# Kernel optimization log

Hardware: AMD Instinct MI355X
Metric: run time of the kernel (lower is better)

## Reference

```python
import jax, jax.numpy as jnp
import numpy as np

N = 20000
IN_C = 512
HID = 64
H1 = 8
OUT_C = 256
E = 320000
NEG_SLOPE = 0.2


def gat_conv(x, src, dst, W, a_src, a_dst, b, concat):
    # PyG GATConv (shared lin for src/dst), inference mode (no dropout).
    H, C = a_src.shape
    h = (x @ W).reshape(N, H, C)                      # [N,H,C]
    alpha_src = (h * a_src[None]).sum(-1)             # [N,H]
    alpha_dst = (h * a_dst[None]).sum(-1)             # [N,H]
    alpha = jax.nn.leaky_relu(alpha_src[src] + alpha_dst[dst], NEG_SLOPE)  # [E,H]
    # segment softmax over incoming edges of each dst node
    amax = jax.ops.segment_max(alpha, dst, num_segments=N)
    amax = jnp.where(jnp.isfinite(amax), amax, 0.0)
    ex = jnp.exp(alpha - amax[dst])
    denom = jax.ops.segment_sum(ex, dst, num_segments=N)
    coef = ex / (denom[dst] + 1e-16)                  # [E,H]
    msg = h[src] * coef[:, :, None]                   # [E,H,C]
    out = jax.ops.segment_sum(msg, dst, num_segments=N)  # [N,H,C]
    out = out.reshape(N, H * C) if concat else out.mean(axis=1)
    return out + b


def setup_inputs() -> dict:
    key = jax.random.key(0)
    ks = jax.random.split(key, 10)
    x = jax.random.normal(ks[0], (N, IN_C), dtype=jnp.float32)
    edge_index = jax.random.randint(ks[1], (2, E), 0, N, dtype=jnp.int32)
    s1 = 1.0 / np.sqrt(IN_C)
    s2 = 1.0 / np.sqrt(HID * H1)
    W1 = jax.random.uniform(ks[2], (IN_C, H1 * HID), jnp.float32, -s1, s1)
    att_src1 = jax.random.uniform(ks[3], (H1, HID), jnp.float32, -s1, s1)
    att_dst1 = jax.random.uniform(ks[4], (H1, HID), jnp.float32, -s1, s1)
    b1 = jnp.zeros((H1 * HID,), jnp.float32)
    W2 = jax.random.uniform(ks[5], (H1 * HID, OUT_C), jnp.float32, -s2, s2)
    att_src2 = jax.random.uniform(ks[6], (1, OUT_C), jnp.float32, -s2, s2)
    att_dst2 = jax.random.uniform(ks[7], (1, OUT_C), jnp.float32, -s2, s2)
    b2 = jnp.zeros((OUT_C,), jnp.float32)
    return {"x": x, "edge_index": edge_index, "W1": W1, "att_src1": att_src1,
            "att_dst1": att_dst1, "b1": b1, "W2": W2, "att_src2": att_src2,
            "att_dst2": att_dst2, "b2": b2}


def reference(x, edge_index, W1, att_src1, att_dst1, b1, W2, att_src2, att_dst2, b2):
    # add self-loops (PyG GATConv default add_self_loops=True)
    loop = jnp.arange(N, dtype=edge_index.dtype)
    src = jnp.concatenate([edge_index[0], loop])
    dst = jnp.concatenate([edge_index[1], loop])
    h = gat_conv(x, src, dst, W1, att_src1, att_dst1, b1, concat=True)
    h = jax.nn.elu(h)
    out = gat_conv(h, src, dst, W2, att_src2, att_dst2, b2, concat=False)
    return jax.nn.log_softmax(out, axis=1)
```

## Files before the change

### kernel.cpp

```cpp
#include <hip/hip_runtime.h>
#include <math.h>

#define N_NODES 20000
#define IN_CH   512
#define HID_TOT 512
#define OUT_CH  256
#define N_EDGE  320000
#define TOT_EDGE (N_EDGE + N_NODES)

typedef __attribute__((ext_vector_type(8))) short short8;
typedef __attribute__((ext_vector_type(4))) float f32x4;
typedef __attribute__((ext_vector_type(2))) float f32x2;

__device__ __forceinline__ ushort f2bf(float f) {
    union { float f; unsigned u; } v; v.f = f;
    unsigned u = v.u;
    return (ushort)((u + 0x7fffu + ((u >> 16) & 1u)) >> 16);
}

__device__ __forceinline__ void glds16(const ushort* g, ushort* l) {
    __builtin_amdgcn_global_load_lds(
        (const __attribute__((address_space(1))) void*)g,
        (__attribute__((address_space(3))) void*)l, 16, 0, 0);
}

__device__ __forceinline__ float lrelu(float a) { return fmaxf(a, 0.2f * a); }

#define NA_BLK (N_NODES * IN_CH / 4 / 256)
#define NB_BLK ((IN_CH / 64) * (HID_TOT / 4))
#define NC_BLK ((HID_TOT / 64) * (OUT_CH / 4))
#define NZ_BLK ((N_NODES + 255) / 256)
__global__ __launch_bounds__(256) void prep_kernel(const float* __restrict__ x,
                                                   ushort* __restrict__ xb,
                                                   const float* __restrict__ W1,
                                                   ushort* __restrict__ w1t,
                                                   const float* __restrict__ W2,
                                                   ushort* __restrict__ w2t,
                                                   int* __restrict__ counts,
                                                   float* __restrict__ as2,
                                                   float* __restrict__ ad2) {
    int b = blockIdx.x;
    int t = threadIdx.x;
    if (b < NA_BLK) {
        int i = b * 256 + t;
        float4 v = *(const float4*)&x[(size_t)i * 4];
        ushort4 o = make_ushort4(f2bf(v.x), f2bf(v.y), f2bf(v.z), f2bf(v.w));
        *(ushort4*)&xb[(size_t)i * 4] = o;
    } else if (b < NA_BLK + NB_BLK) {
        int bb = b - NA_BLK;
        int k = (bb & 7) * 64 + (t & 63);
        int n = (bb >> 3) * 4 + (t >> 6);
        w1t[(size_t)n * IN_CH + k] = f2bf(W1[(size_t)k * HID_TOT + n]);
    } else if (b < NA_BLK + NB_BLK + NC_BLK) {
        int bb = b - NA_BLK - NB_BLK;
        int k = (bb & 7) * 64 + (t & 63);
        int n = (bb >> 3) * 4 + (t >> 6);
        w2t[(size_t)n * HID_TOT + k] = f2bf(W2[(size_t)k * OUT_CH + n]);
    } else {
        int i = (b - NA_BLK - NB_BLK - NC_BLK) * 256 + t;
        if (i < N_NODES) { counts[i] = 0; as2[i] = 0.f; ad2[i] = 0.f; }
    }
}

__global__ void hist_kernel(const int* __restrict__ ei, int* __restrict__ counts) {
    int e = blockIdx.x * blockDim.x + threadIdx.x;
    if (e >= TOT_EDGE) return;
    int d = (e < N_EDGE) ? ei[N_EDGE + e] : (e - N_EDGE);
    atomicAdd(&counts[d], 1);
}

__global__ __launch_bounds__(1024) void scan_kernel(const int* __restrict__ counts,
                                                    int* __restrict__ offsets,
                                                    int* __restrict__ cursors) {
    const int C = (N_NODES + 1023) / 1024;
    int t = threadIdx.x;
    int lane = t & 63, wid = t >> 6;
    int base = t * C;
    int sum = 0;
#pragma unroll
    for (int i = 0; i < C; i++) {
        int idx = base + i;
        if (idx < N_NODES) sum += counts[idx];
    }
    int val = sum;
#pragma unroll
    for (int off = 1; off < 64; off <<= 1) {
        int y = __shfl_up(val, off);
        if (lane >= off) val += y;
    }
    __shared__ int wsum[16], woff[16], stotal;
    if (lane == 63) wsum[wid] = val;
    __syncthreads();
    if (t == 0) {
        int r = 0;
        for (int w = 0; w < 16; w++) { woff[w] = r; r += wsum[w]; }
        stotal = r;
    }
    __syncthreads();
    int running = woff[wid] + (val - sum);
#pragma unroll
    for (int i = 0; i < C; i++) {
        int idx = base + i;
        if (idx < N_NODES) {
            offsets[idx] = running;
            cursors[idx] = running;
            running += counts[idx];
        }
    }
    if (t == 0) offsets[N_NODES] = stotal;
}

__global__ void scatter_kernel(const int* __restrict__ ei, int* __restrict__ cursors,
                               int* __restrict__ srcs) {
    int e = blockIdx.x * blockDim.x + threadIdx.x;
    if (e >= TOT_EDGE) return;
    int s, d;
    if (e < N_EDGE) { s = ei[e]; d = ei[N_EDGE + e]; } else { s = e - N_EDGE; d = s; }
    int pos = atomicAdd(&cursors[d], 1);
    srcs[pos] = s;
}

__global__ __launch_bounds__(256, 2) void gemm_mfma_kernel(const ushort* __restrict__ A,
                                                           const ushort* __restrict__ Bt,
                                                           unsigned char* __restrict__ Cf8,
                                                           const float* __restrict__ asrc,
                                                           const float* __restrict__ adst,
                                                           float* __restrict__ as_out,
                                                           float* __restrict__ ad_out,
                                                           int M, int N, int K, int layer1) {
    __shared__ ushort As[128 * 64];
    __shared__ ushort Bs[128 * 64];
    int t = threadIdx.x;
    int lane = t & 63;
    int wave = t >> 6;
    int wr = (wave >> 1) * 64;
    int wc = (wave & 1) * 64;
    int bm = blockIdx.y * 128, bn = blockIdx.x * 128;
    int q = lane >> 4, l15 = lane & 15;

    const ushort* Aptr[4]; ushort* Alds[4];
    const ushort* Bptr[4]; ushort* Blds[4];
#pragma unroll
    for (int k = 0; k < 4; k++) {
        int c = t + 256 * k;
        int r = c >> 3, kqs = c & 7;
        int kqg = kqs ^ (r & 7);
        int ar = bm + r; if (ar >= M) ar = M - 1;
        Aptr[k] = A + (size_t)ar * K + kqg * 8;
        Alds[k] = &As[c * 8];
        Bptr[k] = Bt + (size_t)(bn + r) * K + kqg * 8;
        Blds[k] = &Bs[c * 8];
    }

    f32x4 acc[4][4];
#pragma unroll
    for (int i = 0; i < 4; i++)
#pragma unroll
        for (int j = 0; j < 4; j++) acc[i][j] = f32x4{0.f, 0.f, 0.f, 0.f};

    for (int k0 = 0; k0 < K; k0 += 64) {
        __syncthreads();
        glds16(Aptr[0] + k0, Alds[0]);
        glds16(Aptr[1] + k0, Alds[1]);
        glds16(Aptr[2] + k0, Alds[2]);
        glds16(Aptr[3] + k0, Alds[3]);
        glds16(Bptr[0] + k0, Blds[0]);
        glds16(Bptr[1] + k0, Blds[1]);
        glds16(Bptr[2] + k0, Blds[2]);
        glds16(Bptr[3] + k0, Blds[3]);
        __syncthreads();

#pragma unroll
        for (int s = 0; s < 2; s++) {
            int kq = s * 4 + q;
            short8 af[4], bf[4];
#pragma unroll
            for (int i = 0; i < 4; i++) {
                int row = wr + i * 16 + l15;
                int slot = kq ^ (row & 7);
                af[i] = *(const short8*)&As[row * 64 + slot * 8];
            }
#pragma unroll
            for (int j = 0; j < 4; j++) {
                int row = wc + j * 16 + l15;
                int slot = kq ^ (row & 7);
                bf[j] = *(const short8*)&Bs[row * 64 + slot * 8];
            }
#pragma unroll
            for (int i = 0; i < 4; i++)
#pragma unroll
                for (int j = 0; j < 4; j++)
                    acc[i][j] = __builtin_amdgcn_mfma_f32_16x16x32_bf16(af[i], bf[j], acc[i][j], 0, 0, 0);
        }
    }

    float av[4], dv[4];
#pragma unroll
    for (int j = 0; j < 4; j++) {
        int cg = bn + wc + j * 16 + l15;
        av[j] = asrc[cg];
        dv[j] = adst[cg];
    }
    float ps[4][4], pd[4][4];
#pragma unroll
    for (int i = 0; i < 4; i++)
#pragma unroll
        for (int r = 0; r < 4; r++) {
            float p = 0.f, d = 0.f;
#pragma unroll
            for (int j = 0; j < 4; j++) {
                p = fmaf(acc[i][j][r], av[j], p);
                d = fmaf(acc[i][j][r], dv[j], d);
            }
            ps[i][r] = p; pd[i][r] = d;
        }
#pragma unroll
    for (int off = 1; off < 16; off <<= 1) {
#pragma unroll
        for (int i = 0; i < 4; i++)
#pragma unroll
            for (int r = 0; r < 4; r++) {
                ps[i][r] += __shfl_xor(ps[i][r], off);
                pd[i][r] += __shfl_xor(pd[i][r], off);
            }
    }

    int hidx = blockIdx.x * 2 + (wave & 1);
#pragma unroll
    for (int i = 0; i < 4; i++) {
#pragma unroll
        for (int r = 0; r < 4; r++) {
            int rg = bm + wr + i * 16 + q * 4 + r;
            if (rg < M) {
#pragma unroll
                for (int j = 0; j < 4; j++) {
                    int cg = bn + wc + j * 16 + l15;
                    int w8 = __builtin_amdgcn_cvt_pk_fp8_f32(acc[i][j][r], acc[i][j][r], 0, false);
                    Cf8[(size_t)rg * N + cg] = (unsigned char)(w8 & 0xff);
                }
                if (l15 == 0) {
                    if (layer1) {
                        as_out[hidx * N_NODES + rg] = ps[i][r];
                        ad_out[hidx * N_NODES + rg] = pd[i][r];
                    } else {
                        atomicAdd(&as_out[rg], ps[i][r]);
                        atomicAdd(&ad_out[rg], pd[i][r]);
                    }
                }
            }
        }
    }
}

__global__ __launch_bounds__(64) void agg1_kernel(const unsigned char* __restrict__ h1f,
                                                  const float* __restrict__ as1,
                                                  const float* __restrict__ ad1,
                                                  const int* __restrict__ offsets,
                                                  const int* __restrict__ srcs,
                                                  const float* __restrict__ b1,
                                                  ushort* __restrict__ h1ab) {
    int b = blockIdx.x;
    int head = b & 7;
    int grp = b >> 3;
    int lane = threadIdx.x;
    int sub = lane >> 3;
    int l8 = lane & 7;
    int v = grp * 8 + sub;
    int cofs = head * 64 + l8 * 8;
    const unsigned char* hb = h1f + cofs;
    const float* as1h = as1 + head * N_NODES;
    int s = offsets[v], e = offsets[v + 1];
    float adv = ad1[head * N_NODES + v];

    float denom = 0.f;
    float acc[8];
#pragma unroll
    for (int k = 0; k < 8; k++) acc[k] = 0.f;

    int i = s;
    for (; i + 4 <= e; i += 4) {
        int sn[4];
#pragma unroll
        for (int j = 0; j < 4; j++) sn[j] = srcs[i + j];
        uint2 r[4];
#pragma unroll
        for (int j = 0; j < 4; j++)
            r[j] = *(const uint2*)&hb[(size_t)sn[j] * HID_TOT];
        float w[4];
#pragma unroll
        for (int j = 0; j < 4; j++) {
            float a = lrelu(as1h[sn[j]] + adv);
            w[j] = __expf(a);
            denom += w[j];
        }
#pragma unroll
        for (int j = 0; j < 4; j++) {
            f32x2 pa = __builtin_amdgcn_cvt_pk_f32_fp8(r[j].x, false);
            f32x2 pb = __builtin_amdgcn_cvt_pk_f32_fp8(r[j].x, true);
            f32x2 pc = __builtin_amdgcn_cvt_pk_f32_fp8(r[j].y, false);
            f32x2 pdd = __builtin_amdgcn_cvt_pk_f32_fp8(r[j].y, true);
            acc[0] = fmaf(w[j], pa.x, acc[0]); acc[1] = fmaf(w[j], pa.y, acc[1]);
            acc[2] = fmaf(w[j], pb.x, acc[2]); acc[3] = fmaf(w[j], pb.y, acc[3]);
            acc[4] = fmaf(w[j], pc.x, acc[4]); acc[5] = fmaf(w[j], pc.y, acc[5]);
            acc[6] = fmaf(w[j], pdd.x, acc[6]); acc[7] = fmaf(w[j], pdd.y, acc[7]);
        }
    }
    for (; i < e; i++) {
        int sn = srcs[i];
        uint2 r = *(const uint2*)&hb[(size_t)sn * HID_TOT];
        float a = lrelu(as1h[sn] + adv);
        float w = __expf(a);
        denom += w;
        f32x2 pa = __builtin_amdgcn_cvt_pk_f32_fp8(r.x, false);
        f32x2 pb = __builtin_amdgcn_cvt_pk_f32_fp8(r.x, true);
        f32x2 pc = __builtin_amdgcn_cvt_pk_f32_fp8(r.y, false);
        f32x2 pdd = __builtin_amdgcn_cvt_pk_f32_fp8(r.y, true);
        acc[0] = fmaf(w, pa.x, acc[0]); acc[1] = fmaf(w, pa.y, acc[1]);
        acc[2] = fmaf(w, pb.x, acc[2]); acc[3] = fmaf(w, pb.y, acc[3]);
        acc[4] = fmaf(w, pc.x, acc[4]); acc[5] = fmaf(w, pc.y, acc[5]);
        acc[6] = fmaf(w, pdd.x, acc[6]); acc[7] = fmaf(w, pdd.y, acc[7]);
    }

    float inv = 1.f / (denom + 1e-16f);
    short8 ov;
#pragma unroll
    for (int k = 0; k < 8; k++) {
        float o = acc[k] * inv + b1[cofs + k];
        o = (o > 0.f) ? o : expm1f(o);
        ov[k] = (short)f2bf(o);
    }
    *(short8*)&h1ab[(size_t)v * HID_TOT + cofs] = ov;
}

__global__ __launch_bounds__(64) void agg2_kernel(const unsigned char* __restrict__ h2f,
                                                  const float* __restrict__ as2,
                                                  const float* __restrict__ ad2,
                                                  const int* __restrict__ offsets,
                                                  const int* __restrict__ srcs,
                                                  const float* __restrict__ b2,
                                                  float* __restrict__ out) {
    int lane = threadIdx.x;
    int sub = lane >> 5;
    int l32 = lane & 31;
    int v = blockIdx.x * 2 + sub;
    int c8 = l32 * 8;
    const unsigned char* hb = h2f + c8;
    int s = offsets[v], e = offsets[v + 1];
    float adv = ad2[v];

    float denom = 0.f;
    float acc[8];
#pragma unroll
    for (int k = 0; k < 8; k++) acc[k] = 0.f;

    int i = s;
    for (; i + 4 <= e; i += 4) {
        int sn[4];
#pragma unroll
        for (int j = 0; j < 4; j++) sn[j] = srcs[i + j];
        uint2 r[4];
#pragma unroll
        for (int j = 0; j < 4; j++)
            r[j] = *(const uint2*)&hb[(size_t)sn[j] * OUT_CH];
        float w[4];
#pragma unroll
        for (int j = 0; j < 4; j++) {
            float a = lrelu(as2[sn[j]] + adv);
            w[j] = __expf(a);
            denom += w[j];
        }
#pragma unroll
        for (int j = 0; j < 4; j++) {
            f32x2 pa = __builtin_amdgcn_cvt_pk_f32_fp8(r[j].x, false);
            f32x2 pb = __builtin_amdgcn_cvt_pk_f32_fp8(r[j].x, true);
            f32x2 pc = __builtin_amdgcn_cvt_pk_f32_fp8(r[j].y, false);
            f32x2 pdd = __builtin_amdgcn_cvt_pk_f32_fp8(r[j].y, true);
            acc[0] = fmaf(w[j], pa.x, acc[0]); acc[1] = fmaf(w[j], pa.y, acc[1]);
            acc[2] = fmaf(w[j], pb.x, acc[2]); acc[3] = fmaf(w[j], pb.y, acc[3]);
            acc[4] = fmaf(w[j], pc.x, acc[4]); acc[5] = fmaf(w[j], pc.y, acc[5]);
            acc[6] = fmaf(w[j], pdd.x, acc[6]); acc[7] = fmaf(w[j], pdd.y, acc[7]);
        }
    }
    for (; i < e; i++) {
        int sn = srcs[i];
        uint2 r = *(const uint2*)&hb[(size_t)sn * OUT_CH];
        float a = lrelu(as2[sn] + adv);
        float w = __expf(a);
        denom += w;
        f32x2 pa = __builtin_amdgcn_cvt_pk_f32_fp8(r.x, false);
        f32x2 pb = __builtin_amdgcn_cvt_pk_f32_fp8(r.x, true);
        f32x2 pc = __builtin_amdgcn_cvt_pk_f32_fp8(r.y, false);
        f32x2 pdd = __builtin_amdgcn_cvt_pk_f32_fp8(r.y, true);
        acc[0] = fmaf(w, pa.x, acc[0]); acc[1] = fmaf(w, pa.y, acc[1]);
        acc[2] = fmaf(w, pb.x, acc[2]); acc[3] = fmaf(w, pb.y, acc[3]);
        acc[4] = fmaf(w, pc.x, acc[4]); acc[5] = fmaf(w, pc.y, acc[5]);
        acc[6] = fmaf(w, pdd.x, acc[6]); acc[7] = fmaf(w, pdd.y, acc[7]);
    }

    float inv = 1.f / (denom + 1e-16f);
    float xv[8];
#pragma unroll
    for (int k = 0; k < 8; k++) xv[k] = acc[k] * inv + b2[c8 + k];

    float mm = xv[0];
#pragma unroll
    for (int k = 1; k < 8; k++) mm = fmaxf(mm, xv[k]);
#pragma unroll
    for (int off = 1; off < 32; off <<= 1) mm = fmaxf(mm, __shfl_xor(mm, off));
    float sum = 0.f;
#pragma unroll
    for (int k = 0; k < 8; k++) sum += __expf(xv[k] - mm);
#pragma unroll
    for (int off = 1; off < 32; off <<= 1) sum += __shfl_xor(sum, off);
    float ls = logf(sum);
    float4 o0, o1;
    o0.x = xv[0] - mm - ls; o0.y = xv[1] - mm - ls;
    o0.z = xv[2] - mm - ls; o0.w = xv[3] - mm - ls;
    o1.x = xv[4] - mm - ls; o1.y = xv[5] - mm - ls;
    o1.z = xv[6] - mm - ls; o1.w = xv[7] - mm - ls;
    *(float4*)&out[(size_t)v * OUT_CH + c8] = o0;
    *(float4*)&out[(size_t)v * OUT_CH + c8 + 4] = o1;
}

static inline size_t align256(size_t x) { return (x + 255) & ~(size_t)255; }

extern "C" void kernel_launch(void* const* d_in, const int* in_sizes, int n_in,
                              void* d_out, int out_size, void* d_ws, size_t ws_size,
                              hipStream_t stream) {
    const float* x    = (const float*)d_in[0];
    const int*   ei   = (const int*)d_in[1];
    const float* W1   = (const float*)d_in[2];
    const float* as1w = (const float*)d_in[3];
    const float* ad1w = (const float*)d_in[4];
    const float* b1   = (const float*)d_in[5];
    const float* W2   = (const float*)d_in[6];
    const float* as2w = (const float*)d_in[7];
    const float* ad2w = (const float*)d_in[8];
    const float* b2   = (const float*)d_in[9];
    float* out = (float*)d_out;

    char* p = (char*)d_ws;
    unsigned char* h1f = (unsigned char*)p; p += align256((size_t)N_NODES * HID_TOT);
    unsigned char* h2f = (unsigned char*)p; p += align256((size_t)N_NODES * OUT_CH);
    ushort* xb   = (ushort*)p; p += align256(sizeof(ushort) * (size_t)N_NODES * IN_CH);
    ushort* h1ab = xb;
    ushort* w1t  = (ushort*)p; p += align256(sizeof(ushort) * (size_t)IN_CH * HID_TOT);
    ushort* w2t  = (ushort*)p; p += align256(sizeof(ushort) * (size_t)HID_TOT * OUT_CH);
    float* as1  = (float*)p; p += align256(sizeof(float) * (size_t)N_NODES * 8);
    float* ad1  = (float*)p; p += align256(sizeof(float) * (size_t)N_NODES * 8);
    float* as2  = (float*)p; p += align256(sizeof(float) * (size_t)N_NODES);
    float* ad2  = (float*)p; p += align256(sizeof(float) * (size_t)N_NODES);
    int* counts  = (int*)p; p += align256(sizeof(int) * (size_t)N_NODES);
    int* offsets = (int*)p; p += align256(sizeof(int) * (size_t)(N_NODES + 1));
    int* cursors = (int*)p; p += align256(sizeof(int) * (size_t)N_NODES);
    int* srcs    = (int*)p; p += align256(sizeof(int) * (size_t)TOT_EDGE);

    prep_kernel<<<NA_BLK + NB_BLK + NC_BLK + NZ_BLK, 256, 0, stream>>>(
        x, xb, W1, w1t, W2, w2t, counts, as2, ad2);

    int eb = (TOT_EDGE + 255) / 256;
    hist_kernel<<<eb, 256, 0, stream>>>(ei, counts);
    scan_kernel<<<1, 1024, 0, stream>>>(counts, offsets, cursors);
    scatter_kernel<<<eb, 256, 0, stream>>>(ei, cursors, srcs);

    gemm_mfma_kernel<<<dim3(HID_TOT / 128, (N_NODES + 127) / 128), 256, 0, stream>>>(
        xb, w1t, h1f, as1w, ad1w, as1, ad1, N_NODES, HID_TOT, IN_CH, 1);
    agg1_kernel<<<2500 * 8, 64, 0, stream>>>(h1f, as1, ad1, offsets, srcs, b1, h1ab);

    gemm_mfma_kernel<<<dim3(OUT_CH / 128, (N_NODES + 127) / 128), 256, 0, stream>>>(
        h1ab, w2t, h2f, as2w, ad2w, as2, ad2, N_NODES, OUT_CH, HID_TOT, 0);
    agg2_kernel<<<N_NODES / 2, 64, 0, stream>>>(h2f, as2, ad2, offsets, srcs, b2, out);
}
```

Measured before the change: 271.4 us.

## Precompute per-edge attention weights in padded CSR and vectorize aggregation loads

Pads each node's CSR segment to a multiple of 4 with dummy edges, stores destinations alongside sources, and adds separate kernels that precompute exp(leaky_relu) edge weights for both layers. The aggregation kernels then read weights and source indices with vector loads and unroll by 8 instead of gathering attention scalars and computing exp per edge. Layer-1 attention scores are also stored node-major so one edge can fetch all 8 heads at once. In exchange it adds two extra kernels, a padding pass, and extra edge-weight memory traffic.

```diff
diff --git a/kernel.cpp b/kernel.cpp
--- a/kernel.cpp
+++ b/kernel.cpp
@@ -7,6 +7,7 @@
 #define OUT_CH  256
 #define N_EDGE  320000
 #define TOT_EDGE (N_EDGE + N_NODES)
+#define EPAD    400000
 
 typedef __attribute__((ext_vector_type(8))) short short8;
 typedef __attribute__((ext_vector_type(4))) float f32x4;
@@ -80,7 +81,7 @@
 #pragma unroll
     for (int i = 0; i < C; i++) {
         int idx = base + i;
-        if (idx < N_NODES) sum += counts[idx];
+        if (idx < N_NODES) sum += (counts[idx] + 3) & ~3;
     }
     int val = sum;
 #pragma unroll
@@ -104,20 +105,29 @@
         if (idx < N_NODES) {
             offsets[idx] = running;
             cursors[idx] = running;
-            running += counts[idx];
+            running += (counts[idx] + 3) & ~3;
         }
     }
     if (t == 0) offsets[N_NODES] = stotal;
 }
 
 __global__ void scatter_kernel(const int* __restrict__ ei, int* __restrict__ cursors,
-                               int* __restrict__ srcs) {
+                               int* __restrict__ srcs, int* __restrict__ dsts) {
     int e = blockIdx.x * blockDim.x + threadIdx.x;
     if (e >= TOT_EDGE) return;
     int s, d;
     if (e < N_EDGE) { s = ei[e]; d = ei[N_EDGE + e]; } else { s = e - N_EDGE; d = s; }
     int pos = atomicAdd(&cursors[d], 1);
     srcs[pos] = s;
+    dsts[pos] = d;
+}
+
+__global__ void pad_kernel(const int* __restrict__ cursors, const int* __restrict__ offsets,
+                           int* __restrict__ srcs, int* __restrict__ dsts) {
+    int v = blockIdx.x * blockDim.x + threadIdx.x;
+    if (v >= N_NODES) return;
+    int a = cursors[v], b = offsets[v + 1];
+    for (int p = a; p < b; p++) { srcs[p] = 0; dsts[p] = -1; }
 }
 
 __global__ __launch_bounds__(256, 2) void gemm_mfma_kernel(const ushort* __restrict__ A,
@@ -240,8 +250,8 @@
                 }
                 if (l15 == 0) {
                     if (layer1) {
-                        as_out[hidx * N_NODES + rg] = ps[i][r];
-                        ad_out[hidx * N_NODES + rg] = pd[i][r];
+                        as_out[rg * 8 + hidx] = ps[i][r];
+                        ad_out[rg * 8 + hidx] = pd[i][r];
                     } else {
                         atomicAdd(&as_out[rg], ps[i][r]);
                         atomicAdd(&ad_out[rg], pd[i][r]);
@@ -252,9 +262,52 @@
     }
 }
 
-__global__ __launch_bounds__(64) void agg1_kernel(const unsigned char* __restrict__ h1f,
+__global__ __launch_bounds__(256) void wk1_kernel(const int* __restrict__ srcs,
+                                                  const int* __restrict__ dsts,
                                                   const float* __restrict__ as1,
                                                   const float* __restrict__ ad1,
+                                                  const int* __restrict__ offsets,
+                                                  float* __restrict__ w1) {
+    int pos = blockIdx.x * 256 + threadIdx.x;
+    int tot = offsets[N_NODES];
+    if (pos >= tot) return;
+    int d = dsts[pos];
+    if (d < 0) {
+#pragma unroll
+        for (int h = 0; h < 8; h++) w1[h * EPAD + pos] = 0.f;
+        return;
+    }
+    int s = srcs[pos];
+    float4 a0 = *(const float4*)&as1[(size_t)s * 8];
+    float4 a1 = *(const float4*)&as1[(size_t)s * 8 + 4];
+    float4 d0 = *(const float4*)&ad1[(size_t)d * 8];
+    float4 d1 = *(const float4*)&ad1[(size_t)d * 8 + 4];
+    w1[0 * EPAD + pos] = __expf(lrelu(a0.x + d0.x));
+    w1[1 * EPAD + pos] = __expf(lrelu(a0.y + d0.y));
+    w1[2 * EPAD + pos] = __expf(lrelu(a0.z + d0.z));
+    w1[3 * EPAD + pos] = __expf(lrelu(a0.w + d0.w));
+    w1[4 * EPAD + pos] = __expf(lrelu(a1.x + d1.x));
+    w1[5 * EPAD + pos] = __expf(lrelu(a1.y + d1.y));
+    w1[6 * EPAD + pos] = __expf(lrelu(a1.z + d1.z));
+    w1[7 * EPAD + pos] = __expf(lrelu(a1.w + d1.w));
+}
+
+__global__ __launch_bounds__(256) void wk2_kernel(const int* __restrict__ srcs,
+                                                  const int* __restrict__ dsts,
+                                                  const float* __restrict__ as2,
+                                                  const float* __restrict__ ad2,
+                                                  const int* __restrict__ offsets,
+                                                  float* __restrict__ w2) {
+    int pos = blockIdx.x * 256 + threadIdx.x;
+    int tot = offsets[N_NODES];
+    if (pos >= tot) return;
+    int d = dsts[pos];
+    if (d < 0) { w2[pos] = 0.f; return; }
+    w2[pos] = __expf(lrelu(as2[srcs[pos]] + ad2[d]));
+}
+
+__global__ __launch_bounds__(64) void agg1_kernel(const unsigned char* __restrict__ h1f,
+                                                  const float* __restrict__ w1,
                                                   const int* __restrict__ offsets,
                                                   const int* __restrict__ srcs,
                                                   const float* __restrict__ b1,
@@ -268,9 +321,8 @@
     int v = grp * 8 + sub;
     int cofs = head * 64 + l8 * 8;
     const unsigned char* hb = h1f + cofs;
-    const float* as1h = as1 + head * N_NODES;
+    const float* wh = w1 + head * EPAD;
     int s = offsets[v], e = offsets[v + 1];
-    float adv = ad1[head * N_NODES + v];
 
     float denom = 0.f;
     float acc[8];
@@ -278,47 +330,55 @@
     for (int k = 0; k < 8; k++) acc[k] = 0.f;
 
     int i = s;
-    for (; i + 4 <= e; i += 4) {
-        int sn[4];
-#pragma unroll
-        for (int j = 0; j < 4; j++) sn[j] = srcs[i + j];
+    for (; i + 8 <= e; i += 8) {
+        int4 s0 = *(const int4*)&srcs[i];
+        int4 s1 = *(const int4*)&srcs[i + 4];
+        float4 w0 = *(const float4*)&wh[i];
+        float4 w1v = *(const float4*)&wh[i + 4];
+        uint2 r[8];
+        r[0] = *(const uint2*)&hb[(size_t)s0.x * HID_TOT];
+        r[1] = *(const uint2*)&hb[(size_t)s0.y * HID_TOT];
+        r[2] = *(const uint2*)&hb[(size_t)s0.z * HID_TOT];
+        r[3] = *(const uint2*)&hb[(size_t)s0.w * HID_TOT];
+        r[4] = *(const uint2*)&hb[(size_t)s1.x * HID_TOT];
+        r[5] = *(const uint2*)&hb[(size_t)s1.y * HID_TOT];
+        r[6] = *(const uint2*)&hb[(size_t)s1.z * HID_TOT];
+        r[7] = *(const uint2*)&hb[(size_t)s1.w * HID_TOT];
+        float ww[8] = {w0.x, w0.y, w0.z, w0.w, w1v.x, w1v.y, w1v.z, w1v.w};
+        denom += (w0.x + w0.y) + (w0.z + w0.w) + (w1v.x + w1v.y) + (w1v.z + w1v.w);
+#pragma unroll
+        for (int j = 0; j < 8; j++) {
+            f32x2 pa = __builtin_amdgcn_cvt_pk_f32_fp8(r[j].x, false);
+            f32x2 pb = __builtin_amdgcn_cvt_pk_f32_fp8(r[j].x, true);
+            f32x2 pc = __builtin_amdgcn_cvt_pk_f32_fp8(r[j].y, false);
+            f32x2 pdd = __builtin_amdgcn_cvt_pk_f32_fp8(r[j].y, true);
+            acc[0] = fmaf(ww[j], pa.x, acc[0]); acc[1] = fmaf(ww[j], pa.y, acc[1]);
+            acc[2] = fmaf(ww[j], pb.x, acc[2]); acc[3] = fmaf(ww[j], pb.y, acc[3]);
+            acc[4] = fmaf(ww[j], pc.x, acc[4]); acc[5] = fmaf(ww[j], pc.y, acc[5]);
+            acc[6] = fmaf(ww[j], pdd.x, acc[6]); acc[7] = fmaf(ww[j], pdd.y, acc[7]);
+        }
+    }
+    if (i < e) {
+        int4 s0 = *(const int4*)&srcs[i];
+        float4 w0 = *(const float4*)&wh[i];
         uint2 r[4];
-#pragma unroll
-        for (int j = 0; j < 4; j++)
-            r[j] = *(const uint2*)&hb[(size_t)sn[j] * HID_TOT];
-        float w[4];
-#pragma unroll
-        for (int j = 0; j < 4; j++) {
-            float a = lrelu(as1h[sn[j]] + adv);
-            w[j] = __expf(a);
-            denom += w[j];
-        }
+        r[0] = *(const uint2*)&hb[(size_t)s0.x * HID_TOT];
+        r[1] = *(const uint2*)&hb[(size_t)s0.y * HID_TOT];
+        r[2] = *(const uint2*)&hb[(size_t)s0.z * HID_TOT];
+        r[3] = *(const uint2*)&hb[(size_t)s0.w * HID_TOT];
+        float ww[4] = {w0.x, w0.y, w0.z, w0.w};
+        denom += (w0.x + w0.y) + (w0.z + w0.w);
 #pragma unroll
         for (int j = 0; j < 4; j++) {
             f32x2 pa = __builtin_amdgcn_cvt_pk_f32_fp8(r[j].x, false);
             f32x2 pb = __builtin_amdgcn_cvt_pk_f32_fp8(r[j].x, true);
             f32x2 pc = __builtin_amdgcn_cvt_pk_f32_fp8(r[j].y, false);
             f32x2 pdd = __builtin_amdgcn_cvt_pk_f32_fp8(r[j].y, true);
-            acc[0] = fmaf(w[j], pa.x, acc[0]); acc[1] = fmaf(w[j], pa.y, acc[1]);
-            acc[2] = fmaf(w[j], pb.x, acc[2]); acc[3] = fmaf(w[j], pb.y, acc[3]);
-            acc[4] = fmaf(w[j], pc.x, acc[4]); acc[5] = fmaf(w[j], pc.y, acc[5]);
-            acc[6] = fmaf(w[j], pdd.x, acc[6]); acc[7] = fmaf(w[j], pdd.y, acc[7]);
-        }
-    }
-    for (; i < e; i++) {
-        int sn = srcs[i];
-        uint2 r = *(const uint2*)&hb[(size_t)sn * HID_TOT];
-        float a = lrelu(as1h[sn] + adv);
-        float w = __expf(a);
-        denom += w;
-        f32x2 pa = __builtin_amdgcn_cvt_pk_f32_fp8(r.x, false);
-        f32x2 pb = __builtin_amdgcn_cvt_pk_f32_fp8(r.x, true);
-        f32x2 pc = __builtin_amdgcn_cvt_pk_f32_fp8(r.y, false);
-        f32x2 pdd = __builtin_amdgcn_cvt_pk_f32_fp8(r.y, true);
-        acc[0] = fmaf(w, pa.x, acc[0]); acc[1] = fmaf(w, pa.y, acc[1]);
-        acc[2] = fmaf(w, pb.x, acc[2]); acc[3] = fmaf(w, pb.y, acc[3]);
-        acc[4] = fmaf(w, pc.x, acc[4]); acc[5] = fmaf(w, pc.y, acc[5]);
-        acc[6] = fmaf(w, pdd.x, acc[6]); acc[7] = fmaf(w, pdd.y, acc[7]);
+            acc[0] = fmaf(ww[j], pa.x, acc[0]); acc[1] = fmaf(ww[j], pa.y, acc[1]);
+            acc[2] = fmaf(ww[j], pb.x, acc[2]); acc[3] = fmaf(ww[j], pb.y, acc[3]);
+            acc[4] = fmaf(ww[j], pc.x, acc[4]); acc[5] = fmaf(ww[j], pc.y, acc[5]);
+            acc[6] = fmaf(ww[j], pdd.x, acc[6]); acc[7] = fmaf(ww[j], pdd.y, acc[7]);
+        }
     }
 
     float inv = 1.f / (denom + 1e-16f);
@@ -333,8 +393,7 @@
 }
 
 __global__ __launch_bounds__(64) void agg2_kernel(const unsigned char* __restrict__ h2f,
-                                                  const float* __restrict__ as2,
-                                                  const float* __restrict__ ad2,
+                                                  const float* __restrict__ w2,
                                                   const int* __restrict__ offsets,
                                                   const int* __restrict__ srcs,
                                                   const float* __restrict__ b2,
@@ -346,7 +405,6 @@
     int c8 = l32 * 8;
     const unsigned char* hb = h2f + c8;
     int s = offsets[v], e = offsets[v + 1];
-    float adv = ad2[v];
 
     float denom = 0.f;
     float acc[8];
@@ -354,47 +412,55 @@
     for (int k = 0; k < 8; k++) acc[k] = 0.f;
 
     int i = s;
-    for (; i + 4 <= e; i += 4) {
-        int sn[4];
-#pragma unroll
-        for (int j = 0; j < 4; j++) sn[j] = srcs[i + j];
+    for (; i + 8 <= e; i += 8) {
+        int4 s0 = *(const int4*)&srcs[i];
+        int4 s1 = *(const int4*)&srcs[i + 4];
+        float4 w0 = *(const float4*)&w2[i];
+        float4 w1v = *(const float4*)&w2[i + 4];
+        uint2 r[8];
+        r[0] = *(const uint2*)&hb[(size_t)s0.x * OUT_CH];
+        r[1] = *(const uint2*)&hb[(size_t)s0.y * OUT_CH];
+        r[2] = *(const uint2*)&hb[(size_t)s0.z * OUT_CH];
+        r[3] = *(const uint2*)&hb[(size_t)s0.w * OUT_CH];
+        r[4] = *(const uint2*)&hb[(size_t)s1.x * OUT_CH];
+        r[5] = *(const uint2*)&hb[(size_t)s1.y * OUT_CH];
+        r[6] = *(const uint2*)&hb[(size_t)s1.z * OUT_CH];
+        r[7] = *(const uint2*)&hb[(size_t)s1.w * OUT_CH];
+        float ww[8] = {w0.x, w0.y, w0.z, w0.w, w1v.x, w1v.y, w1v.z, w1v.w};
+        denom += (w0.x + w0.y) + (w0.z + w0.w) + (w1v.x + w1v.y) + (w1v.z + w1v.w);
+#pragma unroll
+        for (int j = 0; j < 8; j++) {
+            f32x2 pa = __builtin_amdgcn_cvt_pk_f32_fp8(r[j].x, false);
+            f32x2 pb = __builtin_amdgcn_cvt_pk_f32_fp8(r[j].x, true);
+            f32x2 pc = __builtin_amdgcn_cvt_pk_f32_fp8(r[j].y, false);
+            f32x2 pdd = __builtin_amdgcn_cvt_pk_f32_fp8(r[j].y, true);
+            acc[0] = fmaf(ww[j], pa.x, acc[0]); acc[1] = fmaf(ww[j], pa.y, acc[1]);
+            acc[2] = fmaf(ww[j], pb.x, acc[2]); acc[3] = fmaf(ww[j], pb.y, acc[3]);
+            acc[4] = fmaf(ww[j], pc.x, acc[4]); acc[5] = fmaf(ww[j], pc.y, acc[5]);
+            acc[6] = fmaf(ww[j], pdd.x, acc[6]); acc[7] = fmaf(ww[j], pdd.y, acc[7]);
+        }
+    }
+    if (i < e) {
+        int4 s0 = *(const int4*)&srcs[i];
+        float4 w0 = *(const float4*)&w2[i];
         uint2 r[4];
-#pragma unroll
-        for (int j = 0; j < 4; j++)
-            r[j] = *(const uint2*)&hb[(size_t)sn[j] * OUT_CH];
-        float w[4];
-#pragma unroll
-        for (int j = 0; j < 4; j++) {
-            float a = lrelu(as2[sn[j]] + adv);
-            w[j] = __expf(a);
-            denom += w[j];
-        }
+        r[0] = *(const uint2*)&hb[(size_t)s0.x * OUT_CH];
+        r[1] = *(const uint2*)&hb[(size_t)s0.y * OUT_CH];
+        r[2] = *(const uint2*)&hb[(size_t)s0.z * OUT_CH];
+        r[3] = *(const uint2*)&hb[(size_t)s0.w * OUT_CH];
+        float ww[4] = {w0.x, w0.y, w0.z, w0.w};
+        denom += (w0.x + w0.y) + (w0.z + w0.w);
 #pragma unroll
         for (int j = 0; j < 4; j++) {
             f32x2 pa = __builtin_amdgcn_cvt_pk_f32_fp8(r[j].x, false);
             f32x2 pb = __builtin_amdgcn_cvt_pk_f32_fp8(r[j].x, true);
             f32x2 pc = __builtin_amdgcn_cvt_pk_f32_fp8(r[j].y, false);
             f32x2 pdd = __builtin_amdgcn_cvt_pk_f32_fp8(r[j].y, true);
-            acc[0] = fmaf(w[j], pa.x, acc[0]); acc[1] = fmaf(w[j], pa.y, acc[1]);
-            acc[2] = fmaf(w[j], pb.x, acc[2]); acc[3] = fmaf(w[j], pb.y, acc[3]);
-            acc[4] = fmaf(w[j], pc.x, acc[4]); acc[5] = fmaf(w[j], pc.y, acc[5]);
-            acc[6] = fmaf(w[j], pdd.x, acc[6]); acc[7] = fmaf(w[j], pdd.y, acc[7]);
-        }
-    }
-    for (; i < e; i++) {
-        int sn = srcs[i];
-        uint2 r = *(const uint2*)&hb[(size_t)sn * OUT_CH];
-        float a = lrelu(as2[sn] + adv);
-        float w = __expf(a);
-        denom += w;
-        f32x2 pa = __builtin_amdgcn_cvt_pk_f32_fp8(r.x, false);
-        f32x2 pb = __builtin_amdgcn_cvt_pk_f32_fp8(r.x, true);
-        f32x2 pc = __builtin_amdgcn_cvt_pk_f32_fp8(r.y, false);
-        f32x2 pdd = __builtin_amdgcn_cvt_pk_f32_fp8(r.y, true);
-        acc[0] = fmaf(w, pa.x, acc[0]); acc[1] = fmaf(w, pa.y, acc[1]);
-        acc[2] = fmaf(w, pb.x, acc[2]); acc[3] = fmaf(w, pb.y, acc[3]);
-        acc[4] = fmaf(w, pc.x, acc[4]); acc[5] = fmaf(w, pc.y, acc[5]);
-        acc[6] = fmaf(w, pdd.x, acc[6]); acc[7] = fmaf(w, pdd.y, acc[7]);
+            acc[0] = fmaf(ww[j], pa.x, acc[0]); acc[1] = fmaf(ww[j], pa.y, acc[1]);
+            acc[2] = fmaf(ww[j], pb.x, acc[2]); acc[3] = fmaf(ww[j], pb.y, acc[3]);
+            acc[4] = fmaf(ww[j], pc.x, acc[4]); acc[5] = fmaf(ww[j], pc.y, acc[5]);
+            acc[6] = fmaf(ww[j], pdd.x, acc[6]); acc[7] = fmaf(ww[j], pdd.y, acc[7]);
+        }
     }
 
     float inv = 1.f / (denom + 1e-16f);
@@ -453,7 +519,10 @@
     int* counts  = (int*)p; p += align256(sizeof(int) * (size_t)N_NODES);
     int* offsets = (int*)p; p += align256(sizeof(int) * (size_t)(N_NODES + 1));
     int* cursors = (int*)p; p += align256(sizeof(int) * (size_t)N_NODES);
-    int* srcs    = (int*)p; p += align256(sizeof(int) * (size_t)TOT_EDGE);
+    int* srcs    = (int*)p; p += align256(sizeof(int) * (size_t)EPAD);
+    int* dsts    = (int*)p; p += align256(sizeof(int) * (size_t)EPAD);
+    float* w1    = (float*)p; p += align256(sizeof(float) * (size_t)EPAD * 8);
+    float* w2    = (float*)p; p += align256(sizeof(float) * (size_t)EPAD);
 
     prep_kernel<<<NA_BLK + NB_BLK + NC_BLK + NZ_BLK, 256, 0, stream>>>(
         x, xb, W1, w1t, W2, w2t, counts, as2, ad2);
@@ -461,13 +530,17 @@
     int eb = (TOT_EDGE + 255) / 256;
     hist_kernel<<<eb, 256, 0, stream>>>(ei, counts);
     scan_kernel<<<1, 1024, 0, stream>>>(counts, offsets, cursors);
-    scatter_kernel<<<eb, 256, 0, stream>>>(ei, cursors, srcs);
-
+    scatter_kernel<<<eb, 256, 0, stream>>>(ei, cursors, srcs, dsts);
+    pad_kernel<<<(N_NODES + 255) / 256, 256, 0, stream>>>(cursors, offsets, srcs, dsts);
+
+    int wb = (EPAD + 255) / 256;
     gemm_mfma_kernel<<<dim3(HID_TOT / 128, (N_NODES + 127) / 128), 256, 0, stream>>>(
         xb, w1t, h1f, as1w, ad1w, as1, ad1, N_NODES, HID_TOT, IN_CH, 1);
-    agg1_kernel<<<2500 * 8, 64, 0, stream>>>(h1f, as1, ad1, offsets, srcs, b1, h1ab);
+    wk1_kernel<<<wb, 256, 0, stream>>>(srcs, dsts, as1, ad1, offsets, w1);
+    agg1_kernel<<<2500 * 8, 64, 0, stream>>>(h1f, w1, offsets, srcs, b1, h1ab);
 
     gemm_mfma_kernel<<<dim3(OUT_CH / 128, (N_NODES + 127) / 128), 256, 0, stream>>>(
         h1ab, w2t, h2f, as2w, ad2w, as2, ad2, N_NODES, OUT_CH, HID_TOT, 0);
-    agg2_kernel<<<N_NODES / 2, 64, 0, stream>>>(h2f, as2, ad2, offsets, srcs, b2, out);
-}
+    wk2_kernel<<<wb, 256, 0, stream>>>(srcs, dsts, as2, ad2, offsets, w2);
+    agg2_kernel<<<N_NODES / 2, 64, 0, stream>>>(h2f, w2, offsets, srcs, b2, out);
+}
```

After: 284.9 us. 5.0% more time.
